# Kernel optimization log

Hardware: AMD Instinct MI355X
Metric: run time of the kernel (lower is better)

Reference implementation:

```python
import jax, jax.numpy as jnp
import numpy as np

HID, XD, ZD, K = 512, 128, 64, 3
B, T = 64, 1024

def setup_inputs() -> dict:
    key = jax.random.key(0)
    ks = jax.random.split(key, 10)
    s = lambda *d: 1.0 / np.sqrt(d[0])
    return {
        "x_seq": jax.random.normal(ks[0], (B, T, XD), jnp.float32),
        "conv_w": jax.random.normal(ks[1], (K, XD, HID), jnp.float32) * (1.0/np.sqrt(K*XD)),
        "conv_b": jnp.zeros((HID,), jnp.float32),
        "Wx": jax.random.normal(ks[2], (HID, 4*HID), jnp.float32) * (1.0/np.sqrt(HID)),
        "Wh": jax.random.normal(ks[3], (HID, 4*HID), jnp.float32) * (1.0/np.sqrt(HID)),
        "b": jnp.zeros((4*HID,), jnp.float32),
        "W1": jax.random.normal(ks[4], (HID, HID), jnp.float32) * (1.0/np.sqrt(HID)),
        "b1": jnp.zeros((HID,), jnp.float32),
        "W2": jax.random.normal(ks[5], (HID, 2*ZD), jnp.float32) * (1.0/np.sqrt(HID)),
        "b2": jnp.zeros((2*ZD,), jnp.float32),
    }

def _forward(x_seq, conv_w, conv_b, Wx, Wh, b, W1, b1, W2, b2):
    # Conv1D, SAME padding: (B, T, x_dim) -> (B, T, HID)
    conv = jax.lax.conv_general_dilated(
        x_seq, conv_w, window_strides=(1,), padding="SAME",
        dimension_numbers=("NWC", "WIO", "NWC")) + conv_b

    def step(carry, x_t):
        c, h = carry
        # flax LSTMCell: gates i,f,g,o; input dense (no bias) + hidden dense (bias)
        z = x_t @ Wx + h @ Wh + b  # (B, 4*HID)
        i, f, g, o = jnp.split(z, 4, axis=-1)
        i, f, o = jax.nn.sigmoid(i), jax.nn.sigmoid(f), jax.nn.sigmoid(o)
        g = jnp.tanh(g)
        c_new = f * c + i * g
        h_new = o * jnp.tanh(c_new)
        return (c_new, h_new), h_new

    c0 = jnp.zeros((conv.shape[0], HID), conv.dtype)
    h0 = jnp.zeros((conv.shape[0], HID), conv.dtype)
    _, h_seq = jax.lax.scan(step, (c0, h0), jnp.swapaxes(conv, 0, 1))  # (T, B, HID)
    h_seq = jnp.swapaxes(h_seq, 0, 1)  # (B, T, HID)

    # per-step 2-layer MLP head, applied vectorized over (B, T)
    x = jax.nn.relu(h_seq @ W1 + b1)
    out = x @ W2 + b2  # (B, T, 2*ZD)
    mu, log_sigma = jnp.split(out, 2, axis=-1)
    return mu, log_sigma

def reference(x_seq, conv_w, conv_b, Wx, Wh, b, W1, b1, W2, b2):
    return _forward(x_seq, conv_w, conv_b, Wx, Wh, b, W1, b1, W2, b2)
```

## Files before the change

### kernel.cpp

```cpp
#include <hip/hip_runtime.h>
#include <math.h>

typedef unsigned short u16;
typedef unsigned int   u32;
typedef unsigned long long u64;
typedef _Float16 f16;
typedef __attribute__((ext_vector_type(8))) _Float16 f16x8;
typedef __attribute__((ext_vector_type(4))) float    f32x4;

#define T_SEQ 1024
#define NB    64
#define HID   512
#define KC    384
#define G4    2048
#define MR    (NB*T_SEQ)
#define ZD2   128

__device__ __align__(16) f16   g_xwin[(size_t)MR*KC];
__device__ __align__(16) f16   g_cwxt[(size_t)G4*KC];
__device__              float  g_bb[G4];
__device__ __align__(16) f16   g_whT[(size_t)G4*HID];
__device__ __align__(16) f16   g_w1T[(size_t)HID*HID];
__device__ __align__(16) f16   g_w2T[(size_t)ZD2*HID];
__device__              float  g_b1f[HID];
__device__              float  g_b2f[ZD2];
__device__ __align__(16) float g_XW[(size_t)MR*G4];
__device__ __align__(16) f16   g_hseq[(size_t)MR*HID];
__device__ __align__(16) f16   g_tmp1[(size_t)MR*HID];
__device__ __align__(16) u64   g_hstep[(size_t)(T_SEQ+1)*NB*128];
__device__              int    g_flags[T_SEQ*64];
__device__              int    g_in_fp32;

__device__ inline float bf2f(u16 u){ union{u32 i; float f;} v; v.i = ((u32)u)<<16; return v.f; }
__device__ inline u16  f2bf(float f){ union{u32 i; float f;} v; v.f = f; u32 u = v.i;
                                      return (u16)((u + 0x7fffu + ((u>>16)&1u))>>16); }
__device__ inline float load_in(const void* p, size_t i){
  return g_in_fp32 ? ((const float*)p)[i] : bf2f(((const u16*)p)[i]);
}
__device__ inline float fsig(float x){
  return __builtin_amdgcn_rcpf(1.f + __builtin_amdgcn_exp2f(-1.44269504f*x));
}
__device__ inline float ftanh(float x){
  x = fminf(fmaxf(x, -10.f), 10.f);
  float e = __builtin_amdgcn_exp2f(2.88539008f*x);
  return (e - 1.f) * __builtin_amdgcn_rcpf(e + 1.f);
}

__global__ void k_probe(const void* x){
  __shared__ int cnt;
  if (threadIdx.x == 0) cnt = 0;
  __syncthreads();
  int loc = 0;
  for (int i = threadIdx.x; i < 4096; i += 256){
    float a = fabsf(bf2f(((const u16*)x)[i]));
    if (a > 0.01f && a < 10.f) loc++;
  }
  atomicAdd(&cnt, loc);
  __syncthreads();
  if (threadIdx.x == 0) g_in_fp32 = (cnt < 3276) ? 1 : 0;
}

__global__ void k_init(const void* b1, const void* b2){
  int i = blockIdx.x*256 + threadIdx.x;
  if (i < HID)        g_b1f[i] = load_in(b1, i);
  if (i < ZD2)        g_b2f[i] = load_in(b2, i);
  if (i < T_SEQ*64)   g_flags[i] = 0;
  if (i < NB*128)     g_hstep[i] = 0ULL;
}

__global__ void k_combine(const void* conv_w, const void* conv_b, const void* Wx, const void* b){
  int j  = blockIdx.x*256 + threadIdx.x;
  int kc = blockIdx.y;
  float acc = 0.f;
  if (kc < KC){
    for (int m = 0; m < HID; ++m)
      acc += load_in(conv_w, (size_t)kc*HID + m) * load_in(Wx, (size_t)m*G4 + j);
    g_cwxt[(size_t)j*KC + kc] = (f16)acc;
  } else {
    for (int m = 0; m < HID; ++m)
      acc += load_in(conv_b, m) * load_in(Wx, (size_t)m*G4 + j);
    g_bb[j] = acc + load_in(b, j);
  }
}

__device__ inline void trans_body(const void* src, f16* dst, int R, int C){
  size_t i = (size_t)blockIdx.x*256 + threadIdx.x;
  if (i >= (size_t)R*C) return;
  int c = (int)(i / (size_t)R), r = (int)(i % (size_t)R);
  dst[i] = (f16)load_in(src, (size_t)r*C + c);
}
__global__ void k_trans_wh(const void* Wh){ trans_body(Wh, g_whT, HID, G4); }
__global__ void k_trans_w1(const void* W1){ trans_body(W1, g_w1T, HID, HID); }
__global__ void k_trans_w2(const void* W2){ trans_body(W2, g_w2T, HID, ZD2); }

__global__ void k_xwin(const void* x){
  size_t i = (size_t)blockIdx.x*256 + threadIdx.x;
  if (i >= (size_t)MR*KC) return;
  int row = (int)(i / KC), kc = (int)(i % KC);
  int k = kc >> 7, c = kc & 127;
  int b = row >> 10, t = row & 1023;
  int ts = t - 1 + k;
  float v = 0.f;
  if (ts >= 0 && ts < T_SEQ) v = load_in(x, ((size_t)b*T_SEQ + ts)*128 + c);
  g_xwin[i] = (f16)v;
}

template<int MODE, int K>
__device__ inline void gemm_body(const f16* __restrict__ A, const f16* __restrict__ BT,
                                 const float* __restrict__ bias, void* __restrict__ C, int N){
  const int tid = threadIdx.x;
  const int w = tid >> 6, lane = tid & 63;
  const int q = lane >> 4, ln = lane & 15;
  const int n0 = blockIdx.x * 128;
  const int m0 = blockIdx.y * 64;
  const f16* ap = A + (size_t)(m0 + w*16 + ln)*K + q*8;
  const f16* bp = BT + (size_t)(n0 + ln)*K + q*8;
  f32x4 acc[8] = {};
  #pragma unroll 4
  for (int k = 0; k < K; k += 32){
    f16x8 af = *(const f16x8*)(ap + k);
    #pragma unroll
    for (int nt = 0; nt < 8; ++nt){
      f16x8 bf = *(const f16x8*)(bp + (size_t)nt*16*K + k);
      acc[nt] = __builtin_amdgcn_mfma_f32_16x16x32_f16(af, bf, acc[nt], 0, 0, 0);
    }
  }
  const int f32o = g_in_fp32;
  #pragma unroll
  for (int nt = 0; nt < 8; ++nt){
    const int col = n0 + nt*16 + ln;
    const float bv = bias[col];
    #pragma unroll
    for (int r = 0; r < 4; ++r){
      const int row = m0 + w*16 + q*4 + r;
      float v = acc[nt][r] + bv;
      if (MODE == 0){
        ((float*)C)[(size_t)row*N + col] = v;
      } else if (MODE == 1){
        ((f16*)C)[(size_t)row*N + col] = (f16)fmaxf(v, 0.f);
      } else {
        size_t idx = (col < 64) ? ((size_t)row*64 + col)
                                : (4194304UL + (size_t)row*64 + (size_t)(col - 64));
        if (f32o) ((float*)C)[idx] = v;
        else      ((u16*)C)[idx]   = f2bf(v);
      }
    }
  }
}
__global__ __launch_bounds__(256) void k_gemm_xw(){   gemm_body<0,KC >(g_xwin, g_cwxt, g_bb,  g_XW,   G4 ); }
__global__ __launch_bounds__(256) void k_gemm_mlp1(){ gemm_body<1,HID>(g_hseq, g_w1T,  g_b1f, g_tmp1, HID); }
__global__ __launch_bounds__(256) void k_gemm_mlp2(void* out){ gemm_body<2,HID>(g_tmp1, g_w2T, g_b2f, out, ZD2); }

__global__ __launch_bounds__(256) void k_lstm(){
  __shared__ __align__(16) f16 whs[32*520];
  const int g   = blockIdx.x;
  const int tid = threadIdx.x;
  const int w = tid >> 6, lane = tid & 63;
  const int q = lane >> 4, ln = lane & 15;

  for (int idx = tid; idx < 32*HID; idx += 256){
    int r = idx >> 9, k = idx & 511;
    int zcol = (r >> 3)*HID + g*8 + (r & 7);
    whs[r*520 + k] = g_whT[(size_t)zcol*HID + k];
  }
  __syncthreads();

  const int  c8 = ln & 7;
  const bool lo = ln < 8;
  const int  zc0  = (lo ? 0 : HID)       + g*8 + c8;
  const int  zc1  = (lo ? 2*HID : 3*HID) + g*8 + c8;
  const int  colh = g*8 + c8;
  const int  am   = w*16 + ln;
  float c_st[4] = {0.f, 0.f, 0.f, 0.f};

  for (int t = 0; t < T_SEQ; ++t){
    float xwa[4], xwb[4];
    #pragma unroll
    for (int r = 0; r < 4; ++r){
      size_t base = ((size_t)((w*16 + q*4 + r)*T_SEQ + t))*G4;
      xwa[r] = g_XW[base + zc0];
      xwb[r] = g_XW[base + zc1];
    }
    if (t > 0){
      if (tid < 64){
        while (__hip_atomic_load(&g_flags[(t-1)*64 + tid],
                                 __ATOMIC_RELAXED, __HIP_MEMORY_SCOPE_AGENT) == 0) {}
      }
      __syncthreads();
    }
    const u64* hrow = g_hstep + ((size_t)t*NB + am)*128 + q*2;
    u64 hv[32];
    #pragma unroll
    for (int kk = 0; kk < 16; ++kk){
      hv[2*kk]   = __hip_atomic_load(hrow + (size_t)kk*8,     __ATOMIC_RELAXED, __HIP_MEMORY_SCOPE_AGENT);
      hv[2*kk+1] = __hip_atomic_load(hrow + (size_t)kk*8 + 1, __ATOMIC_RELAXED, __HIP_MEMORY_SCOPE_AGENT);
    }
    f32x4 a0 = {0.f,0.f,0.f,0.f}, a1 = {0.f,0.f,0.f,0.f};
    #pragma unroll
    for (int kk = 0; kk < 16; ++kk){
      union { u64 u[2]; f16x8 v; } cvt;
      cvt.u[0] = hv[2*kk]; cvt.u[1] = hv[2*kk+1];
      f16x8 af = cvt.v;
      int k = kk*32;
      f16x8 b0 = *(const f16x8*)&whs[(0*16 + ln)*520 + k + q*8];
      f16x8 b1 = *(const f16x8*)&whs[(1*16 + ln)*520 + k + q*8];
      a0 = __builtin_amdgcn_mfma_f32_16x16x32_f16(af, b0, a0, 0, 0, 0);
      a1 = __builtin_amdgcn_mfma_f32_16x16x32_f16(af, b1, a1, 0, 0, 0);
    }
    f16 h16v[4];
    #pragma unroll
    for (int r = 0; r < 4; ++r){
      float z0 = a0[r] + xwa[r];
      float z1 = a1[r] + xwb[r];
      float zf = __shfl_xor(z0, 8, 64);
      float zo = __shfl_xor(z1, 8, 64);
      float iv = fsig(z0);
      float fv = fsig(zf);
      float gv = ftanh(z1);
      float ov = fsig(zo);
      float cn = fv*c_st[r] + iv*gv;
      c_st[r] = cn;
      float hvf = ov*ftanh(cn);
      f16 h16 = (f16)hvf;
      h16v[r] = h16;
      u32 me = (u32)__builtin_bit_cast(u16, h16);
      u32 p1 = me | (((u32)__shfl_xor((int)me, 1, 64)) << 16);
      u32 p2 = (u32)__shfl_xor((int)p1, 2, 64);
      u64 pk = (u64)p1 | ((u64)p2 << 32);
      if (lo && (c8 & 3) == 0){
        int m = w*16 + q*4 + r;
        __hip_atomic_store(g_hstep + ((size_t)(t+1)*NB + m)*128 + (size_t)g*2 + (c8>>2),
                           pk, __ATOMIC_RELAXED, __HIP_MEMORY_SCOPE_AGENT);
      }
    }
    asm volatile("s_waitcnt vmcnt(0)" ::: "memory");
    __syncthreads();
    if (tid == 0)
      __hip_atomic_store(&g_flags[t*64 + g], 1, __ATOMIC_RELAXED, __HIP_MEMORY_SCOPE_AGENT);
    if (lo){
      #pragma unroll
      for (int r = 0; r < 4; ++r){
        int m = w*16 + q*4 + r;
        g_hseq[((size_t)m*T_SEQ + t)*HID + colh] = h16v[r];
      }
    }
  }
}

extern "C" void kernel_launch(void* const* d_in, const int* in_sizes, int n_in,
                              void* d_out, int out_size, void* d_ws, size_t ws_size,
                              hipStream_t stream){
  const void* x      = d_in[0];
  const void* conv_w = d_in[1];
  const void* conv_b = d_in[2];
  const void* Wx     = d_in[3];
  const void* Wh     = d_in[4];
  const void* b      = d_in[5];
  const void* W1     = d_in[6];
  const void* b1     = d_in[7];
  const void* W2     = d_in[8];
  const void* b2     = d_in[9];
  (void)in_sizes; (void)n_in; (void)out_size; (void)d_ws; (void)ws_size;

  hipLaunchKernelGGL(k_probe,   dim3(1),        dim3(256), 0, stream, x);
  hipLaunchKernelGGL(k_init,    dim3(256),      dim3(256), 0, stream, b1, b2);
  hipLaunchKernelGGL(k_combine, dim3(8, 385),   dim3(256), 0, stream, conv_w, conv_b, Wx, b);
  hipLaunchKernelGGL(k_trans_wh,dim3(4096),     dim3(256), 0, stream, Wh);
  hipLaunchKernelGGL(k_trans_w1,dim3(1024),     dim3(256), 0, stream, W1);
  hipLaunchKernelGGL(k_trans_w2,dim3(256),      dim3(256), 0, stream, W2);
  hipLaunchKernelGGL(k_xwin,    dim3(98304),    dim3(256), 0, stream, x);
  hipLaunchKernelGGL(k_gemm_xw, dim3(16, 1024), dim3(256), 0, stream);
  hipLaunchKernelGGL(k_lstm,    dim3(64),       dim3(256), 0, stream);
  hipLaunchKernelGGL(k_gemm_mlp1, dim3(4, 1024), dim3(256), 0, stream);
  hipLaunchKernelGGL(k_gemm_mlp2, dim3(1, 1024), dim3(256), 0, stream, d_out);
}
```

Before: 7.808 ms.

## Restructure LSTM to 32 workgroups with packed fp16 gate inputs and shared hstep

```diff
diff --git a/kernel.cpp b/kernel.cpp
--- a/kernel.cpp
+++ b/kernel.cpp
@@ -15,6 +15,7 @@
 #define G4    2048
 #define MR    (NB*T_SEQ)
 #define ZD2   128
+#define NWG   32
 
 __device__ __align__(16) f16   g_xwin[(size_t)MR*KC];
 __device__ __align__(16) f16   g_cwxt[(size_t)G4*KC];
@@ -24,19 +25,20 @@
 __device__ __align__(16) f16   g_w2T[(size_t)ZD2*HID];
 __device__              float  g_b1f[HID];
 __device__              float  g_b2f[ZD2];
-__device__ __align__(16) float g_XW[(size_t)MR*G4];
-__device__ __align__(16) f16   g_hseq[(size_t)MR*HID];
+__device__ __align__(16) f16   g_xwp[(size_t)NWG*T_SEQ*NB*64];
+__device__ __align__(16) f16   g_hstep[(size_t)(T_SEQ+1)*NB*HID];
 __device__ __align__(16) f16   g_tmp1[(size_t)MR*HID];
-__device__ __align__(16) u64   g_hstep[(size_t)(T_SEQ+1)*NB*128];
-__device__              int    g_flags[T_SEQ*64];
+__device__              int    g_flags[T_SEQ*NWG];
 __device__              int    g_in_fp32;
 
 __device__ inline float bf2f(u16 u){ union{u32 i; float f;} v; v.i = ((u32)u)<<16; return v.f; }
 __device__ inline u16  f2bf(float f){ union{u32 i; float f;} v; v.f = f; u32 u = v.i;
                                       return (u16)((u + 0x7fffu + ((u>>16)&1u))>>16); }
-__device__ inline float load_in(const void* p, size_t i){
-  return g_in_fp32 ? ((const float*)p)[i] : bf2f(((const u16*)p)[i]);
-}
+__device__ inline float load_f(const void* p, size_t i, int f32){
+  return f32 ? ((const float*)p)[i] : bf2f(((const u16*)p)[i]);
+}
+__device__ inline float load_in(const void* p, size_t i){ return load_f(p, i, g_in_fp32); }
+__device__ inline float xwf(u16 v){ return (float)__builtin_bit_cast(f16, v); }
 __device__ inline float fsig(float x){
   return __builtin_amdgcn_rcpf(1.f + __builtin_amdgcn_exp2f(-1.44269504f*x));
 }
@@ -64,34 +66,43 @@
   int i = blockIdx.x*256 + threadIdx.x;
   if (i < HID)        g_b1f[i] = load_in(b1, i);
   if (i < ZD2)        g_b2f[i] = load_in(b2, i);
-  if (i < T_SEQ*64)   g_flags[i] = 0;
-  if (i < NB*128)     g_hstep[i] = 0ULL;
+  if (i < T_SEQ*NWG)  g_flags[i] = 0;
+  if (i < NB*HID/4)   ((u64*)g_hstep)[i] = 0ULL;
 }
 
 __global__ void k_combine(const void* conv_w, const void* conv_b, const void* Wx, const void* b){
   int j  = blockIdx.x*256 + threadIdx.x;
   int kc = blockIdx.y;
+  const int lf = g_in_fp32;
   float acc = 0.f;
   if (kc < KC){
     for (int m = 0; m < HID; ++m)
-      acc += load_in(conv_w, (size_t)kc*HID + m) * load_in(Wx, (size_t)m*G4 + j);
+      acc += load_f(conv_w, (size_t)kc*HID + m, lf) * load_f(Wx, (size_t)m*G4 + j, lf);
     g_cwxt[(size_t)j*KC + kc] = (f16)acc;
   } else {
     for (int m = 0; m < HID; ++m)
-      acc += load_in(conv_b, m) * load_in(Wx, (size_t)m*G4 + j);
-    g_bb[j] = acc + load_in(b, j);
-  }
-}
-
-__device__ inline void trans_body(const void* src, f16* dst, int R, int C){
-  size_t i = (size_t)blockIdx.x*256 + threadIdx.x;
-  if (i >= (size_t)R*C) return;
-  int c = (int)(i / (size_t)R), r = (int)(i % (size_t)R);
-  dst[i] = (f16)load_in(src, (size_t)r*C + c);
-}
-__global__ void k_trans_wh(const void* Wh){ trans_body(Wh, g_whT, HID, G4); }
-__global__ void k_trans_w1(const void* W1){ trans_body(W1, g_w1T, HID, HID); }
-__global__ void k_trans_w2(const void* W2){ trans_body(W2, g_w2T, HID, ZD2); }
+      acc += load_f(conv_b, m, lf) * load_f(Wx, (size_t)m*G4 + j, lf);
+    g_bb[j] = acc + load_f(b, j, lf);
+  }
+}
+
+template<int R, int C>
+__device__ inline void trans_tile(const void* src, f16* dst){
+  __shared__ float tl[32][33];
+  const int tx = threadIdx.x & 31, ty = threadIdx.x >> 5;
+  const int cb = blockIdx.x*32, rb = blockIdx.y*32;
+  const int lf = g_in_fp32;
+  #pragma unroll
+  for (int yo = 0; yo < 32; yo += 8)
+    tl[ty+yo][tx] = load_f(src, (size_t)(rb+ty+yo)*C + cb + tx, lf);
+  __syncthreads();
+  #pragma unroll
+  for (int yo = 0; yo < 32; yo += 8)
+    dst[(size_t)(cb+ty+yo)*R + rb + tx] = (f16)tl[tx][ty+yo];
+}
+__global__ void k_trans_wh(const void* s){ trans_tile<HID, G4 >(s, g_whT); }
+__global__ void k_trans_w1(const void* s){ trans_tile<HID, HID>(s, g_w1T); }
+__global__ void k_trans_w2(const void* s){ trans_tile<HID, ZD2>(s, g_w2T); }
 
 __global__ void k_xwin(const void* x){
   size_t i = (size_t)blockIdx.x*256 + threadIdx.x;
@@ -101,33 +112,35 @@
   int b = row >> 10, t = row & 1023;
   int ts = t - 1 + k;
   float v = 0.f;
-  if (ts >= 0 && ts < T_SEQ) v = load_in(x, ((size_t)b*T_SEQ + ts)*128 + c);
+  if (ts >= 0 && ts < T_SEQ) v = load_f(x, ((size_t)b*T_SEQ + ts)*128 + c, g_in_fp32);
   g_xwin[i] = (f16)v;
 }
 
-template<int MODE, int K>
+template<int MODE, int K, int NT, int AMODE>
 __device__ inline void gemm_body(const f16* __restrict__ A, const f16* __restrict__ BT,
                                  const float* __restrict__ bias, void* __restrict__ C, int N){
   const int tid = threadIdx.x;
   const int w = tid >> 6, lane = tid & 63;
   const int q = lane >> 4, ln = lane & 15;
-  const int n0 = blockIdx.x * 128;
+  const int n0 = blockIdx.x * (NT*16);
   const int m0 = blockIdx.y * 64;
-  const f16* ap = A + (size_t)(m0 + w*16 + ln)*K + q*8;
+  const int rm = m0 + w*16 + ln;
+  const int ar = (AMODE == 1) ? (((rm & 1023) + 1)*64 + (rm >> 10)) : rm;
+  const f16* ap = A + (size_t)ar*K + q*8;
   const f16* bp = BT + (size_t)(n0 + ln)*K + q*8;
-  f32x4 acc[8] = {};
-  #pragma unroll 4
+  f32x4 acc[NT] = {};
+  #pragma unroll 2
   for (int k = 0; k < K; k += 32){
     f16x8 af = *(const f16x8*)(ap + k);
     #pragma unroll
-    for (int nt = 0; nt < 8; ++nt){
+    for (int nt = 0; nt < NT; ++nt){
       f16x8 bf = *(const f16x8*)(bp + (size_t)nt*16*K + k);
       acc[nt] = __builtin_amdgcn_mfma_f32_16x16x32_f16(af, bf, acc[nt], 0, 0, 0);
     }
   }
   const int f32o = g_in_fp32;
   #pragma unroll
-  for (int nt = 0; nt < 8; ++nt){
+  for (int nt = 0; nt < NT; ++nt){
     const int col = n0 + nt*16 + ln;
     const float bv = bias[col];
     #pragma unroll
@@ -135,7 +148,9 @@
       const int row = m0 + w*16 + q*4 + r;
       float v = acc[nt][r] + bv;
       if (MODE == 0){
-        ((float*)C)[(size_t)row*N + col] = v;
+        int t = row & 1023, b = row >> 10;
+        int gw = (col & 511) >> 4, inner = (col >> 9)*16 + (col & 15);
+        g_xwp[(((size_t)gw*T_SEQ + t)*NB + b)*64 + inner] = (f16)v;
       } else if (MODE == 1){
         ((f16*)C)[(size_t)row*N + col] = (f16)fmaxf(v, 0.f);
       } else {
@@ -147,103 +162,88 @@
     }
   }
 }
-__global__ __launch_bounds__(256) void k_gemm_xw(){   gemm_body<0,KC >(g_xwin, g_cwxt, g_bb,  g_XW,   G4 ); }
-__global__ __launch_bounds__(256) void k_gemm_mlp1(){ gemm_body<1,HID>(g_hseq, g_w1T,  g_b1f, g_tmp1, HID); }
-__global__ __launch_bounds__(256) void k_gemm_mlp2(void* out){ gemm_body<2,HID>(g_tmp1, g_w2T, g_b2f, out, ZD2); }
-
-__global__ __launch_bounds__(256) void k_lstm(){
-  __shared__ __align__(16) f16 whs[32*520];
+__global__ __launch_bounds__(256) void k_gemm_xw(){   gemm_body<0,KC, 16,0>(g_xwin,  g_cwxt, g_bb,  nullptr, G4 ); }
+__global__ __launch_bounds__(256) void k_gemm_mlp1(){ gemm_body<1,HID,16,1>(g_hstep, g_w1T,  g_b1f, g_tmp1,  HID); }
+__global__ __launch_bounds__(256) void k_gemm_mlp2(void* out){ gemm_body<2,HID,8,0>(g_tmp1, g_w2T, g_b2f, out, ZD2); }
+
+__global__ __launch_bounds__(256,1) void k_lstm(){
+  __shared__ __align__(16) f16 whs[64*64*8];
   const int g   = blockIdx.x;
   const int tid = threadIdx.x;
   const int w = tid >> 6, lane = tid & 63;
   const int q = lane >> 4, ln = lane & 15;
 
-  for (int idx = tid; idx < 32*HID; idx += 256){
-    int r = idx >> 9, k = idx & 511;
-    int zcol = (r >> 3)*HID + g*8 + (r & 7);
-    whs[r*520 + k] = g_whT[(size_t)zcol*HID + k];
-  }
-  __syncthreads();
-
-  const int  c8 = ln & 7;
-  const bool lo = ln < 8;
-  const int  zc0  = (lo ? 0 : HID)       + g*8 + c8;
-  const int  zc1  = (lo ? 2*HID : 3*HID) + g*8 + c8;
-  const int  colh = g*8 + c8;
-  const int  am   = w*16 + ln;
+  for (int idx = tid; idx < 64*64; idx += 256){
+    int kq = idx >> 6, r = idx & 63;
+    int zcol = (r >> 4)*HID + g*16 + (r & 15);
+    *(f16x8*)&whs[((size_t)kq*64 + r)*8] = *(const f16x8*)&g_whT[(size_t)zcol*HID + (size_t)kq*8];
+  }
+  __syncthreads();
+
   float c_st[4] = {0.f, 0.f, 0.f, 0.f};
+  const u16* xwbase = (const u16*)(g_xwp + (size_t)g*T_SEQ*NB*64) + (size_t)(w*16 + q*4)*64 + ln;
+  const int am = w*16 + ln;
 
   for (int t = 0; t < T_SEQ; ++t){
-    float xwa[4], xwb[4];
-    #pragma unroll
-    for (int r = 0; r < 4; ++r){
-      size_t base = ((size_t)((w*16 + q*4 + r)*T_SEQ + t))*G4;
-      xwa[r] = g_XW[base + zc0];
-      xwb[r] = g_XW[base + zc1];
-    }
-    if (t > 0){
-      if (tid < 64){
-        while (__hip_atomic_load(&g_flags[(t-1)*64 + tid],
-                                 __ATOMIC_RELAXED, __HIP_MEMORY_SCOPE_AGENT) == 0) {}
-      }
-      __syncthreads();
-    }
-    const u64* hrow = g_hstep + ((size_t)t*NB + am)*128 + q*2;
+    u16 xwv[16];
+    {
+      const u16* xp = xwbase + (size_t)t*(NB*64);
+      #pragma unroll
+      for (int kk = 0; kk < 16; ++kk) xwv[kk] = xp[kk*16];
+    }
+    if (t > 0 && tid < NWG){
+      while (__hip_atomic_load(&g_flags[(t-1)*NWG + tid],
+                               __ATOMIC_RELAXED, __HIP_MEMORY_SCOPE_AGENT) == 0) {}
+    }
+    __syncthreads();
+
+    const u64* hrow = (const u64*)(g_hstep + ((size_t)t*NB + am)*HID) + q*2;
     u64 hv[32];
     #pragma unroll
     for (int kk = 0; kk < 16; ++kk){
       hv[2*kk]   = __hip_atomic_load(hrow + (size_t)kk*8,     __ATOMIC_RELAXED, __HIP_MEMORY_SCOPE_AGENT);
       hv[2*kk+1] = __hip_atomic_load(hrow + (size_t)kk*8 + 1, __ATOMIC_RELAXED, __HIP_MEMORY_SCOPE_AGENT);
     }
-    f32x4 a0 = {0.f,0.f,0.f,0.f}, a1 = {0.f,0.f,0.f,0.f};
+
+    f32x4 a0 = {0.f,0.f,0.f,0.f}, a1 = a0, a2 = a0, a3 = a0;
     #pragma unroll
     for (int kk = 0; kk < 16; ++kk){
       union { u64 u[2]; f16x8 v; } cvt;
       cvt.u[0] = hv[2*kk]; cvt.u[1] = hv[2*kk+1];
-      f16x8 af = cvt.v;
-      int k = kk*32;
-      f16x8 b0 = *(const f16x8*)&whs[(0*16 + ln)*520 + k + q*8];
-      f16x8 b1 = *(const f16x8*)&whs[(1*16 + ln)*520 + k + q*8];
-      a0 = __builtin_amdgcn_mfma_f32_16x16x32_f16(af, b0, a0, 0, 0, 0);
-      a1 = __builtin_amdgcn_mfma_f32_16x16x32_f16(af, b1, a1, 0, 0, 0);
-    }
-    f16 h16v[4];
+      const int base = (kk*4 + q)*64*8;
+      f16x8 b0 = *(const f16x8*)&whs[base + (  0 + ln)*8];
+      f16x8 b1 = *(const f16x8*)&whs[base + ( 16 + ln)*8];
+      f16x8 b2 = *(const f16x8*)&whs[base + ( 32 + ln)*8];
+      f16x8 b3 = *(const f16x8*)&whs[base + ( 48 + ln)*8];
+      a0 = __builtin_amdgcn_mfma_f32_16x16x32_f16(cvt.v, b0, a0, 0, 0, 0);
+      a1 = __builtin_amdgcn_mfma_f32_16x16x32_f16(cvt.v, b1, a1, 0, 0, 0);
+      a2 = __builtin_amdgcn_mfma_f32_16x16x32_f16(cvt.v, b2, a2, 0, 0, 0);
+      a3 = __builtin_amdgcn_mfma_f32_16x16x32_f16(cvt.v, b3, a3, 0, 0, 0);
+    }
+
     #pragma unroll
     for (int r = 0; r < 4; ++r){
-      float z0 = a0[r] + xwa[r];
-      float z1 = a1[r] + xwb[r];
-      float zf = __shfl_xor(z0, 8, 64);
-      float zo = __shfl_xor(z1, 8, 64);
-      float iv = fsig(z0);
-      float fv = fsig(zf);
-      float gv = ftanh(z1);
-      float ov = fsig(zo);
+      float zi = a0[r] + xwf(xwv[r*4+0]);
+      float zf = a1[r] + xwf(xwv[r*4+1]);
+      float zg = a2[r] + xwf(xwv[r*4+2]);
+      float zo = a3[r] + xwf(xwv[r*4+3]);
+      float iv = fsig(zi), fv = fsig(zf), gv = ftanh(zg), ov = fsig(zo);
       float cn = fv*c_st[r] + iv*gv;
       c_st[r] = cn;
-      float hvf = ov*ftanh(cn);
-      f16 h16 = (f16)hvf;
-      h16v[r] = h16;
+      f16 h16 = (f16)(ov*ftanh(cn));
       u32 me = (u32)__builtin_bit_cast(u16, h16);
-      u32 p1 = me | (((u32)__shfl_xor((int)me, 1, 64)) << 16);
-      u32 p2 = (u32)__shfl_xor((int)p1, 2, 64);
-      u64 pk = (u64)p1 | ((u64)p2 << 32);
-      if (lo && (c8 & 3) == 0){
+      u32 p  = me | (((u32)__shfl_xor((int)me, 1, 64)) << 16);
+      u64 pk = (u64)p | (((u64)(u32)__shfl_xor((int)p, 2, 64)) << 32);
+      if ((ln & 3) == 0){
         int m = w*16 + q*4 + r;
-        __hip_atomic_store(g_hstep + ((size_t)(t+1)*NB + m)*128 + (size_t)g*2 + (c8>>2),
-                           pk, __ATOMIC_RELAXED, __HIP_MEMORY_SCOPE_AGENT);
+        u64* sp = (u64*)(g_hstep + ((size_t)(t+1)*NB + m)*HID + g*16 + ln);
+        __hip_atomic_store(sp, pk, __ATOMIC_RELAXED, __HIP_MEMORY_SCOPE_AGENT);
       }
     }
     asm volatile("s_waitcnt vmcnt(0)" ::: "memory");
     __syncthreads();
     if (tid == 0)
-      __hip_atomic_store(&g_flags[t*64 + g], 1, __ATOMIC_RELAXED, __HIP_MEMORY_SCOPE_AGENT);
-    if (lo){
-      #pragma unroll
-      for (int r = 0; r < 4; ++r){
-        int m = w*16 + q*4 + r;
-        g_hseq[((size_t)m*T_SEQ + t)*HID + colh] = h16v[r];
-      }
-    }
+      __hip_atomic_store(&g_flags[t*NWG + g], 1, __ATOMIC_RELAXED, __HIP_MEMORY_SCOPE_AGENT);
   }
 }
 
@@ -262,15 +262,15 @@
   const void* b2     = d_in[9];
   (void)in_sizes; (void)n_in; (void)out_size; (void)d_ws; (void)ws_size;
 
-  hipLaunchKernelGGL(k_probe,   dim3(1),        dim3(256), 0, stream, x);
-  hipLaunchKernelGGL(k_init,    dim3(256),      dim3(256), 0, stream, b1, b2);
-  hipLaunchKernelGGL(k_combine, dim3(8, 385),   dim3(256), 0, stream, conv_w, conv_b, Wx, b);
-  hipLaunchKernelGGL(k_trans_wh,dim3(4096),     dim3(256), 0, stream, Wh);
-  hipLaunchKernelGGL(k_trans_w1,dim3(1024),     dim3(256), 0, stream, W1);
-  hipLaunchKernelGGL(k_trans_w2,dim3(256),      dim3(256), 0, stream, W2);
-  hipLaunchKernelGGL(k_xwin,    dim3(98304),    dim3(256), 0, stream, x);
-  hipLaunchKernelGGL(k_gemm_xw, dim3(16, 1024), dim3(256), 0, stream);
-  hipLaunchKernelGGL(k_lstm,    dim3(64),       dim3(256), 0, stream);
-  hipLaunchKernelGGL(k_gemm_mlp1, dim3(4, 1024), dim3(256), 0, stream);
+  hipLaunchKernelGGL(k_probe,    dim3(1),        dim3(256), 0, stream, x);
+  hipLaunchKernelGGL(k_init,     dim3(256),      dim3(256), 0, stream, b1, b2);
+  hipLaunchKernelGGL(k_combine,  dim3(8, 385),   dim3(256), 0, stream, conv_w, conv_b, Wx, b);
+  hipLaunchKernelGGL(k_trans_wh, dim3(64, 16),   dim3(256), 0, stream, Wh);
+  hipLaunchKernelGGL(k_trans_w1, dim3(16, 16),   dim3(256), 0, stream, W1);
+  hipLaunchKernelGGL(k_trans_w2, dim3(4, 16),    dim3(256), 0, stream, W2);
+  hipLaunchKernelGGL(k_xwin,     dim3(98304),    dim3(256), 0, stream, x);
+  hipLaunchKernelGGL(k_gemm_xw,  dim3(8, 1024),  dim3(256), 0, stream);
+  hipLaunchKernelGGL(k_lstm,     dim3(NWG),      dim3(256), 0, stream);
+  hipLaunchKernelGGL(k_gemm_mlp1, dim3(2, 1024), dim3(256), 0, stream);
   hipLaunchKernelGGL(k_gemm_mlp2, dim3(1, 1024), dim3(256), 0, stream, d_out);
 }
```

New measurement: 8.362 ms. 7.1% more time.
